# Kernel tuning notes

Measured on AMD Instinct MI355X. Metric: run time of the kernel, lower is better.

The kernel has to match this reference:

```python
import jax, jax.numpy as jnp
import numpy as np

# Module hyperparameters (init_kwargs)
DIM = 512
NUM_HEADS = 8
ALPHA = 0.5
WS = 2                       # window_size
HEAD_DIM = DIM // NUM_HEADS  # 64
L_HEADS = int(NUM_HEADS * ALPHA)      # 4 low-freq heads
L_DIM = L_HEADS * HEAD_DIM            # 256
H_HEADS = NUM_HEADS - L_HEADS         # 4 high-freq heads
H_DIM = H_HEADS * HEAD_DIM            # 256
SCALE = HEAD_DIM ** -0.5

B, HH, WW = 8, 64, 64  # batch, feature-map height/width


def setup_inputs() -> dict:
    key = jax.random.key(0)
    ks = jax.random.split(key, 7)
    s = 0.02  # weight init scale
    return {
        "x": jax.random.normal(ks[0], (B, HH * WW, DIM), jnp.float32),
        "h_qkv_w": jax.random.normal(ks[1], (DIM, 3 * H_DIM), jnp.float32) * s,
        "h_proj_w": jax.random.normal(ks[2], (H_DIM, H_DIM), jnp.float32) * s,
        "h_proj_b": jnp.zeros((H_DIM,), jnp.float32),
        "l_q_w": jax.random.normal(ks[3], (DIM, L_DIM), jnp.float32) * s,
        "l_kv_w": jax.random.normal(ks[4], (DIM, 2 * L_DIM), jnp.float32) * s,
        "l_proj_w": jax.random.normal(ks[5], (L_DIM, L_DIM), jnp.float32) * s,
        "l_proj_b": jnp.zeros((L_DIM,), jnp.float32),
        "H_in": HH,
        "W_in": WW,
    }


def _hilo_forward(x, h_qkv_w, h_proj_w, h_proj_b, l_q_w, l_kv_w, l_proj_w, l_proj_b, H, W):
    Bx, N, C = x.shape
    xi = x.reshape(Bx, H, W, C)
    hg, wg = H // WS, W // WS
    G = hg * wg  # number of windows

    # ---- Hi-Fi: window-partitioned local attention ----
    # [B, hg, WS, wg, WS, C] -> [B, G, WS*WS, C]
    xw = xi.reshape(Bx, hg, WS, wg, WS, C).transpose(0, 1, 3, 2, 4, 5).reshape(Bx, G, WS * WS, C)
    qkv = (xw @ h_qkv_w).reshape(Bx, G, WS * WS, 3, H_HEADS, HEAD_DIM)
    q, k, v = jnp.moveaxis(qkv, 3, 0)
    attn = jax.nn.softmax(jnp.einsum('bgnhd,bgmhd->bghnm', q, k) * SCALE, axis=-1)
    o = jnp.einsum('bghnm,bgmhd->bgnhd', attn, v).reshape(Bx, hg, wg, WS, WS, H_DIM)
    o = o.transpose(0, 1, 3, 2, 4, 5).reshape(Bx, H, W, H_DIM)
    hifi = o @ h_proj_w + h_proj_b  # [B, H, W, H_DIM]

    # ---- Lo-Fi: global attention over avg-pooled keys/values ----
    q = (x @ l_q_w).reshape(Bx, N, L_HEADS, HEAD_DIM).transpose(0, 2, 1, 3)  # [B, lh, N, d]
    # AvgPool2d(kernel=WS, stride=WS): mean over each WS x WS window
    xp = xi.reshape(Bx, hg, WS, wg, WS, C).mean(axis=(2, 4)).reshape(Bx, G, C)
    kv = (xp @ l_kv_w).reshape(Bx, G, 2, L_HEADS, HEAD_DIM)
    k, v = jnp.moveaxis(kv, 2, 0)  # [B, G, lh, d]
    attn = jax.nn.softmax(jnp.einsum('bhnd,bmhd->bhnm', q, k) * SCALE, axis=-1)
    lo = jnp.einsum('bhnm,bmhd->bnhd', attn, v).reshape(Bx, H, W, L_DIM)
    lofi = lo @ l_proj_w + l_proj_b  # [B, H, W, L_DIM]

    return jnp.concatenate([hifi, lofi], axis=-1).reshape(Bx, N, C)


def reference(x, h_qkv_w, h_proj_w, h_proj_b, l_q_w, l_kv_w, l_proj_w, l_proj_b, H_in, W_in):
    return _hilo_forward(x, h_qkv_w, h_proj_w, h_proj_b, l_q_w, l_kv_w, l_proj_w, l_proj_b, H_in, W_in)
```

## Files before the change

kernel.cpp:

```cpp
#include <hip/hip_runtime.h>


typedef __bf16 bf16;
typedef __attribute__((ext_vector_type(8))) __bf16 bf16x8;
typedef __attribute__((ext_vector_type(4))) __bf16 bf16x4;
typedef __attribute__((ext_vector_type(4))) float f32x4;

#define SCALE 0.125f

__device__ __forceinline__ void gload_lds16(const bf16* g, bf16* l) {
    __builtin_amdgcn_global_load_lds(
        (const __attribute__((address_space(1))) void*)g,
        (__attribute__((address_space(3))) void*)l, 16, 0, 0);
}

template <int BM, int BN, bool OUT_BF16, bool BIAS>
__global__ __launch_bounds__(256, 2) void gemm_nt_k(
    const bf16* __restrict__ A, const bf16* __restrict__ Bm,
    void* __restrict__ C, const float* __restrict__ bias,
    int K, int lda, int ldb, int ldc,
    long sAb, long sBb, long sCb, int nh, long sAh, long sBh, long sCh)
{
    constexpr int BK = 32;
    constexpr int FM = BM / 32;
    constexpr int FN = BN / 32;
    constexpr int AL = BM / 64;
    constexpr int BL = BN / 64;

    __shared__ bf16 As[BM * BK];
    __shared__ bf16 Bs[BN * BK];

    const int tid = threadIdx.x, lane = tid & 63, wv = tid >> 6;
    const int wm = wv >> 1, wn = wv & 1;

    const int z = blockIdx.z;
    const int bz = z / nh, hz = z % nh;
    A  += (size_t)bz * sAb + (size_t)hz * sAh;
    Bm += (size_t)bz * sBb + (size_t)hz * sBh;
    const size_t coff = (size_t)bz * sCb + (size_t)hz * sCh;

    const int rowBase = blockIdx.x * BM;
    const int colBase = blockIdx.y * BN;

    const int lrow = lane >> 2;
    const int lkb  = (((lane & 3) ^ ((lane >> 3) & 3))) * 8;

    f32x4 acc[FM][FN] = {};

    const int nkt = K / BK;
    for (int kt = 0; kt < nkt; ++kt) {
#pragma unroll
        for (int i = 0; i < AL; ++i) {
            const int wl = wv * AL + i;
            const int r  = wl * 16 + lrow;
            gload_lds16(A + (size_t)(rowBase + r) * lda + kt * BK + lkb,
                        &As[wl * 512]);
        }
#pragma unroll
        for (int i = 0; i < BL; ++i) {
            const int wl = wv * BL + i;
            const int r  = wl * 16 + lrow;
            gload_lds16(Bm + (size_t)(colBase + r) * ldb + kt * BK + lkb,
                        &Bs[wl * 512]);
        }
        __syncthreads();

        bf16x8 af[FM], bfr[FN];
#pragma unroll
        for (int fm = 0; fm < FM; ++fm) {
            const int row = wm * (FM * 16) + fm * 16 + (lane & 15);
            const int sl  = (lane >> 4) ^ ((row >> 1) & 3);
            af[fm] = *(const bf16x8*)&As[row * BK + sl * 8];
        }
#pragma unroll
        for (int fn = 0; fn < FN; ++fn) {
            const int row = wn * (FN * 16) + fn * 16 + (lane & 15);
            const int sl  = (lane >> 4) ^ ((row >> 1) & 3);
            bfr[fn] = *(const bf16x8*)&Bs[row * BK + sl * 8];
        }
#pragma unroll
        for (int fm = 0; fm < FM; ++fm)
#pragma unroll
            for (int fn = 0; fn < FN; ++fn)
                acc[fm][fn] = __builtin_amdgcn_mfma_f32_16x16x32_bf16(
                    af[fm], bfr[fn], acc[fm][fn], 0, 0, 0);
        __syncthreads();
    }

#pragma unroll
    for (int fm = 0; fm < FM; ++fm) {
#pragma unroll
        for (int fn = 0; fn < FN; ++fn) {
#pragma unroll
            for (int j = 0; j < 4; ++j) {
                const int row = rowBase + wm * (FM * 16) + fm * 16 + (lane >> 4) * 4 + j;
                const int col = colBase + wn * (FN * 16) + fn * 16 + (lane & 15);
                float v = acc[fm][fn][j];
                if (BIAS) v += bias[col];
                if (OUT_BF16)
                    ((bf16*)C)[coff + (size_t)row * ldc + col] = (bf16)v;
                else
                    ((float*)C)[coff + (size_t)row * ldc + col] = v;
            }
        }
    }
}

__global__ __launch_bounds__(256) void convert_x(const float* __restrict__ x,
                                                 bf16* __restrict__ xb)
{
    const size_t i = ((size_t)blockIdx.x * 256 + threadIdx.x) * 8;
    const float4 a = *(const float4*)(x + i);
    const float4 b = *(const float4*)(x + i + 4);
    bf16x8 o;
    o[0] = (bf16)a.x; o[1] = (bf16)a.y; o[2] = (bf16)a.z; o[3] = (bf16)a.w;
    o[4] = (bf16)b.x; o[5] = (bf16)b.y; o[6] = (bf16)b.z; o[7] = (bf16)b.w;
    *(bf16x8*)(xb + i) = o;
}

__global__ __launch_bounds__(256) void transpose_w(const float* __restrict__ in,
                                                   bf16* __restrict__ out,
                                                   int K, int N)
{
    const int i = blockIdx.x * 256 + threadIdx.x;
    if (i >= K * N) return;
    const int n = i / K, k = i % K;
    out[i] = (bf16)in[(size_t)k * N + n];
}

__global__ __launch_bounds__(256) void avgpool_x(const float* __restrict__ x,
                                                 bf16* __restrict__ xp)
{
    const int i = blockIdx.x * 256 + threadIdx.x;
    const int c4 = i & 127;
    const int g  = (i >> 7) & 1023;
    const int b  = i >> 17;
    const int gy = g >> 5, gx = g & 31;
    const float* base = x + ((size_t)b * 4096 + gy * 128 + gx * 2) * 512 + c4 * 4;
    const float4 a0 = *(const float4*)(base);
    const float4 a1 = *(const float4*)(base + 512);
    const float4 a2 = *(const float4*)(base + 64 * 512);
    const float4 a3 = *(const float4*)(base + 65 * 512);
    bf16x4 o;
    o[0] = (bf16)((a0.x + a1.x + a2.x + a3.x) * 0.25f);
    o[1] = (bf16)((a0.y + a1.y + a2.y + a3.y) * 0.25f);
    o[2] = (bf16)((a0.z + a1.z + a2.z + a3.z) * 0.25f);
    o[3] = (bf16)((a0.w + a1.w + a2.w + a3.w) * 0.25f);
    *(bf16x4*)(xp + ((size_t)b * 1024 + g) * 512 + c4 * 4) = o;
}

__global__ __launch_bounds__(256) void win_attn(const bf16* __restrict__ qkv,
                                                bf16* __restrict__ o_h)
{
    __shared__ float p_lds[4][64];
    const int wv = threadIdx.x >> 6, lane = threadIdx.x & 63;
    const int w = blockIdx.x * 4 + wv;
    const int b = w >> 10, g = w & 1023;
    const int gy = g >> 5, gx = g & 31;
    int t[4];
    t[0] = gy * 128 + gx * 2; t[1] = t[0] + 1; t[2] = t[0] + 64; t[3] = t[0] + 65;

    const int h = lane >> 4, n = (lane >> 2) & 3, m = lane & 3;
    const bf16* qp = qkv + ((size_t)b * 4096 + t[n]) * 768 + h * 64;
    const bf16* kp = qkv + ((size_t)b * 4096 + t[m]) * 768 + 256 + h * 64;
    float s = 0.f;
#pragma unroll
    for (int i = 0; i < 8; ++i) {
        const bf16x8 a = *(const bf16x8*)(qp + i * 8);
        const bf16x8 c = *(const bf16x8*)(kp + i * 8);
#pragma unroll
        for (int j = 0; j < 8; ++j) s += (float)a[j] * (float)c[j];
    }
    s *= SCALE;
    float mx = fmaxf(s, __shfl_xor(s, 1)); mx = fmaxf(mx, __shfl_xor(mx, 2));
    const float e = __expf(s - mx);
    float sum = e + __shfl_xor(e, 1); sum = sum + __shfl_xor(sum, 2);
    p_lds[wv][lane] = e / sum;
    __syncthreads();

#pragma unroll
    for (int hn = 0; hn < 16; ++hn) {
        const int hh = hn >> 2, nn = hn & 3;
        float o = 0.f;
#pragma unroll
        for (int mm = 0; mm < 4; ++mm) {
            const float p = p_lds[wv][hh * 16 + nn * 4 + mm];
            o += p * (float)qkv[((size_t)b * 4096 + t[mm]) * 768 + 512 + hh * 64 + lane];
        }
        o_h[((size_t)b * 4096 + t[nn]) * 256 + hh * 64 + lane] = (bf16)o;
    }
}

__global__ __launch_bounds__(256) void make_kT(const bf16* __restrict__ kv,
                                               bf16* __restrict__ kT)
{
    const int i = blockIdx.x * 256 + threadIdx.x;
    const int e = i & 7, s = (i >> 3) & 7, key = (i >> 6) & 1023;
    const int h = (i >> 16) & 3, b = i >> 18;
    kT[i] = kv[((size_t)(b * 1024 + key)) * 512 + h * 64 + (((s ^ (key & 7)) << 3) | e)];
}

__global__ __launch_bounds__(256) void make_vT(const bf16* __restrict__ kv,
                                               bf16* __restrict__ vT)
{
    const int i = blockIdx.x * 256 + threadIdx.x;
    const int e = i & 7, s = (i >> 3) & 7, c = (i >> 6) & 15;
    const int d = (i >> 10) & 63, h = (i >> 16) & 3, b = i >> 18;
    const int g = c * 64 + (((s ^ (d & 7)) << 3) | e);
    vT[i] = kv[((size_t)(b * 1024 + g)) * 512 + 256 + h * 64 + d];
}

__global__ __launch_bounds__(256, 2) void lofi_attn(
    const bf16* __restrict__ q_l, const bf16* __restrict__ kT,
    const bf16* __restrict__ vT, bf16* __restrict__ lo)
{
    __shared__ bf16 Ks[64][64];
    __shared__ bf16 Vs[64][64];
    __shared__ bf16 Ps[4][16][72];

    const int lane = threadIdx.x & 63, wv = threadIdx.x >> 6;
    const int g16 = lane >> 4, l15 = lane & 15;
    const int bh = blockIdx.y, b = bh >> 2, h = bh & 3;

    const int qrow = blockIdx.x * 64 + wv * 16 + l15;
    const bf16* qbase = q_l + ((size_t)b * 4096 + qrow) * 256 + h * 64;
    const bf16x8 qf0 = *(const bf16x8*)(qbase + g16 * 8);
    const bf16x8 qf1 = *(const bf16x8*)(qbase + 32 + g16 * 8);

    const bf16* kTb = kT + (size_t)bh * 1024 * 64;
    const bf16* vTb = vT + (size_t)bh * 64 * 1024;

    f32x4 of[4] = {};
    float m = -1e30f, l = 0.f;

    for (int kc = 0; kc < 16; ++kc) {
        const int r0 = wv * 16;
#pragma unroll
        for (int i = 0; i < 2; ++i) {
            gload_lds16(kTb + ((size_t)(kc * 64 + r0 + i * 8)) * 64 + lane * 8,
                        &Ks[r0 + i * 8][0]);
            gload_lds16(vTb + ((size_t)(r0 + i * 8 + (lane >> 3))) * 1024
                            + kc * 64 + (lane & 7) * 8,
                        &Vs[r0 + i * 8][0]);
        }
        __syncthreads();

        f32x4 s[4];
#pragma unroll
        for (int nf = 0; nf < 4; ++nf) {
            const int key = nf * 16 + l15;
            const int f = key & 7;
            const bf16x8 ka0 = *(const bf16x8*)&Ks[key][((g16) ^ f) * 8];
            const bf16x8 ka1 = *(const bf16x8*)&Ks[key][((4 + g16) ^ f) * 8];
            f32x4 a = {};
            a = __builtin_amdgcn_mfma_f32_16x16x32_bf16(ka0, qf0, a, 0, 0, 0);
            a = __builtin_amdgcn_mfma_f32_16x16x32_bf16(ka1, qf1, a, 0, 0, 0);
            s[nf] = a;
        }

        float cm = -1e30f;
#pragma unroll
        for (int nf = 0; nf < 4; ++nf)
#pragma unroll
            for (int j = 0; j < 4; ++j) {
                s[nf][j] *= SCALE;
                cm = fmaxf(cm, s[nf][j]);
            }
        cm = fmaxf(cm, __shfl_xor(cm, 16));
        cm = fmaxf(cm, __shfl_xor(cm, 32));
        const float newm = fmaxf(m, cm);
        const float corr = __expf(m - newm);
        float cs = 0.f;
#pragma unroll
        for (int nf = 0; nf < 4; ++nf) {
            bf16x4 pw;
#pragma unroll
            for (int j = 0; j < 4; ++j) {
                const float p = __expf(s[nf][j] - newm);
                cs += p;
                pw[j] = (bf16)p;
            }
            *(bf16x4*)&Ps[wv][l15][nf * 16 + g16 * 4] = pw;
        }
        cs += __shfl_xor(cs, 16);
        cs += __shfl_xor(cs, 32);
        l = l * corr + cs;
        m = newm;

        float corr_t[4];
#pragma unroll
        for (int j = 0; j < 4; ++j) corr_t[j] = __shfl(corr, g16 * 4 + j);
#pragma unroll
        for (int df = 0; df < 4; ++df)
#pragma unroll
            for (int j = 0; j < 4; ++j) of[df][j] *= corr_t[j];

        const bf16x8 pa0 = *(const bf16x8*)&Ps[wv][l15][g16 * 8];
        const bf16x8 pa1 = *(const bf16x8*)&Ps[wv][l15][32 + g16 * 8];
#pragma unroll
        for (int df = 0; df < 4; ++df) {
            const int d = df * 16 + l15;
            const int f = d & 7;
            const bf16x8 vb0 = *(const bf16x8*)&Vs[d][((g16) ^ f) * 8];
            const bf16x8 vb1 = *(const bf16x8*)&Vs[d][((4 + g16) ^ f) * 8];
            of[df] = __builtin_amdgcn_mfma_f32_16x16x32_bf16(pa0, vb0, of[df], 0, 0, 0);
            of[df] = __builtin_amdgcn_mfma_f32_16x16x32_bf16(pa1, vb1, of[df], 0, 0, 0);
        }
        __syncthreads();
    }

    const float linv = 1.0f / l;
    float linv_t[4];
#pragma unroll
    for (int j = 0; j < 4; ++j) linv_t[j] = __shfl(linv, g16 * 4 + j);
    const int orow0 = blockIdx.x * 64 + wv * 16;
#pragma unroll
    for (int df = 0; df < 4; ++df)
#pragma unroll
        for (int j = 0; j < 4; ++j) {
            const int row = orow0 + g16 * 4 + j;
            lo[((size_t)b * 4096 + row) * 256 + h * 64 + df * 16 + l15] =
                (bf16)(of[df][j] * linv_t[j]);
        }
}

extern "C" void kernel_launch(void* const* d_in, const int* in_sizes, int n_in,
                              void* d_out, int out_size, void* d_ws, size_t ws_size,
                              hipStream_t stream)
{
    const float* x        = (const float*)d_in[0];
    const float* h_qkv_w  = (const float*)d_in[1];
    const float* h_proj_w = (const float*)d_in[2];
    const float* h_proj_b = (const float*)d_in[3];
    const float* l_q_w    = (const float*)d_in[4];
    const float* l_kv_w   = (const float*)d_in[5];
    const float* l_proj_w = (const float*)d_in[6];
    const float* l_proj_b = (const float*)d_in[7];
    float* out = (float*)d_out;

    char* ws = (char*)d_ws;
    bf16*  xb    = (bf16*)(ws + 0);
    bf16*  wqkvT = (bf16*)(ws + 33554432);
    bf16*  whpT  = (bf16*)(ws + 34340864);
    bf16*  wlqT  = (bf16*)(ws + 34471936);
    bf16*  wlkvT = (bf16*)(ws + 34734080);
    bf16*  wlpT  = (bf16*)(ws + 35258368);
    bf16*  qkv   = (bf16*)(ws + 35389440);
    bf16*  o_h   = (bf16*)(ws + 85721088);
    bf16*  kT    = (bf16*)(ws + 85721088);
    bf16*  vT    = (bf16*)(ws + 89915392);
    bf16*  q_l   = (bf16*)(ws + 102498304);
    bf16*  xp    = (bf16*)(ws + 119275520);
    bf16*  kv    = (bf16*)(ws + 127664128);
    bf16*  lo    = (bf16*)(ws + 136052736);

    convert_x<<<8192, 256, 0, stream>>>(x, xb);
    transpose_w<<<1536, 256, 0, stream>>>(h_qkv_w, wqkvT, 512, 768);
    transpose_w<<<256, 256, 0, stream>>>(h_proj_w, whpT, 256, 256);
    transpose_w<<<512, 256, 0, stream>>>(l_q_w, wlqT, 512, 256);
    transpose_w<<<1024, 256, 0, stream>>>(l_kv_w, wlkvT, 512, 512);
    transpose_w<<<256, 256, 0, stream>>>(l_proj_w, wlpT, 256, 256);

    gemm_nt_k<128, 128, true, false><<<dim3(256, 6, 1), 256, 0, stream>>>(
        xb, wqkvT, qkv, nullptr, 512, 512, 512, 768, 0, 0, 0, 1, 0, 0, 0);
    win_attn<<<2048, 256, 0, stream>>>(qkv, o_h);
    gemm_nt_k<128, 128, false, true><<<dim3(256, 2, 1), 256, 0, stream>>>(
        o_h, whpT, out, h_proj_b, 256, 256, 256, 512, 0, 0, 0, 1, 0, 0, 0);

    gemm_nt_k<128, 128, true, false><<<dim3(256, 2, 1), 256, 0, stream>>>(
        xb, wlqT, q_l, nullptr, 512, 512, 512, 256, 0, 0, 0, 1, 0, 0, 0);
    avgpool_x<<<4096, 256, 0, stream>>>(x, xp);
    gemm_nt_k<128, 128, true, false><<<dim3(64, 4, 1), 256, 0, stream>>>(
        xp, wlkvT, kv, nullptr, 512, 512, 512, 512, 0, 0, 0, 1, 0, 0, 0);
    make_kT<<<8192, 256, 0, stream>>>(kv, kT);
    make_vT<<<8192, 256, 0, stream>>>(kv, vT);

    lofi_attn<<<dim3(64, 32), 256, 0, stream>>>(q_l, kT, vT, lo);

    gemm_nt_k<128, 128, false, true><<<dim3(256, 2, 1), 256, 0, stream>>>(
        lo, wlpT, out + 256, l_proj_b, 256, 256, 256, 512, 0, 0, 0, 1, 0, 0, 0);
}
```

Measured before the change: 337.2 us.

## Double-buffer lofi attention K/V tiles, double queries per wave, remap blocks per XCD

The lofi attention kernel now double-buffers K/V tiles in LDS, issuing the next chunk's global-to-LDS loads before computing on the current one. This leaves one barrier per iteration instead of two. Each wave handles two 16-row query groups, so each loaded K/V tile is reused twice, and the grid becomes a 1D launch of 1024 blocks mapped so that one XCD's blocks share the same batch-head K/V data. The two K/V transpose kernels are merged into one launch. The cost is more LDS and registers per block, which may reduce occupancy.

```diff
diff --git a/kernel.cpp b/kernel.cpp
--- a/kernel.cpp
+++ b/kernel.cpp
@@ -191,137 +191,171 @@
     }
 }
 
-__global__ __launch_bounds__(256) void make_kT(const bf16* __restrict__ kv,
-                                               bf16* __restrict__ kT)
-{
-    const int i = blockIdx.x * 256 + threadIdx.x;
-    const int e = i & 7, s = (i >> 3) & 7, key = (i >> 6) & 1023;
-    const int h = (i >> 16) & 3, b = i >> 18;
-    kT[i] = kv[((size_t)(b * 1024 + key)) * 512 + h * 64 + (((s ^ (key & 7)) << 3) | e)];
-}
-
-__global__ __launch_bounds__(256) void make_vT(const bf16* __restrict__ kv,
-                                               bf16* __restrict__ vT)
-{
-    const int i = blockIdx.x * 256 + threadIdx.x;
-    const int e = i & 7, s = (i >> 3) & 7, c = (i >> 6) & 15;
-    const int d = (i >> 10) & 63, h = (i >> 16) & 3, b = i >> 18;
-    const int g = c * 64 + (((s ^ (d & 7)) << 3) | e);
-    vT[i] = kv[((size_t)(b * 1024 + g)) * 512 + 256 + h * 64 + d];
+__global__ __launch_bounds__(256) void make_kvT(const bf16* __restrict__ kv,
+                                                bf16* __restrict__ kT,
+                                                bf16* __restrict__ vT)
+{
+    const int idx = blockIdx.x * 256 + threadIdx.x;
+    if (idx < 2097152) {
+        const int i = idx;
+        const int e = i & 7, s = (i >> 3) & 7, key = (i >> 6) & 1023;
+        const int h = (i >> 16) & 3, b = i >> 18;
+        kT[i] = kv[((size_t)(b * 1024 + key)) * 512 + h * 64 + (((s ^ (key & 7)) << 3) | e)];
+    } else {
+        const int i = idx - 2097152;
+        const int e = i & 7, s = (i >> 3) & 7, c = (i >> 6) & 15;
+        const int d = (i >> 10) & 63, h = (i >> 16) & 3, b = i >> 18;
+        const int g = c * 64 + (((s ^ (d & 7)) << 3) | e);
+        vT[i] = kv[((size_t)(b * 1024 + g)) * 512 + 256 + h * 64 + d];
+    }
 }
 
 __global__ __launch_bounds__(256, 2) void lofi_attn(
     const bf16* __restrict__ q_l, const bf16* __restrict__ kT,
     const bf16* __restrict__ vT, bf16* __restrict__ lo)
 {
-    __shared__ bf16 Ks[64][64];
-    __shared__ bf16 Vs[64][64];
+    __shared__ bf16 Ks[2][64][64];
+    __shared__ bf16 Vs[2][64][64];
     __shared__ bf16 Ps[4][16][72];
 
     const int lane = threadIdx.x & 63, wv = threadIdx.x >> 6;
     const int g16 = lane >> 4, l15 = lane & 15;
-    const int bh = blockIdx.y, b = bh >> 2, h = bh & 3;
-
-    const int qrow = blockIdx.x * 64 + wv * 16 + l15;
-    const bf16* qbase = q_l + ((size_t)b * 4096 + qrow) * 256 + h * 64;
-    const bf16x8 qf0 = *(const bf16x8*)(qbase + g16 * 8);
-    const bf16x8 qf1 = *(const bf16x8*)(qbase + 32 + g16 * 8);
-
-    const bf16* kTb = kT + (size_t)bh * 1024 * 64;
-    const bf16* vTb = vT + (size_t)bh * 64 * 1024;
-
-    f32x4 of[4] = {};
-    float m = -1e30f, l = 0.f;
-
+
+    const int bid = blockIdx.x;
+    const int xcd = bid & 7, chunk = bid >> 3;
+    const int bh = xcd * 4 + (chunk >> 5);
+    const int qt = chunk & 31;
+    const int b = bh >> 2, h = bh & 3;
+
+    bf16x8 qf[2][2];
+#pragma unroll
+    for (int qh = 0; qh < 2; ++qh) {
+        const int qrow = qt * 128 + wv * 32 + qh * 16 + l15;
+        const bf16* qbase = q_l + ((size_t)b * 4096 + qrow) * 256 + h * 64;
+        qf[qh][0] = *(const bf16x8*)(qbase + g16 * 8);
+        qf[qh][1] = *(const bf16x8*)(qbase + 32 + g16 * 8);
+    }
+
+    const bf16* kTb = kT + (size_t)bh * 65536;
+    const bf16* vTb = vT + (size_t)bh * 65536;
+
+    f32x4 of[2][4] = {};
+    float m0 = -1e30f, l0 = 0.f, m1 = -1e30f, l1 = 0.f;
+
+    const int r0 = wv * 16;
+    const int vrow = r0 + (lane >> 3);
+    const int vke  = (lane & 7) * 8;
+
+#define STAGE(buf, kc)                                                          \
+    {                                                                           \
+        _Pragma("unroll")                                                       \
+        for (int i = 0; i < 2; ++i) {                                           \
+            gload_lds16(kTb + ((size_t)((kc) * 64 + r0 + i * 8)) * 64 + lane * 8,\
+                        &Ks[buf][r0 + i * 8][0]);                               \
+            gload_lds16(vTb + ((size_t)(vrow + i * 8)) * 1024 + (kc) * 64 + vke,\
+                        &Vs[buf][r0 + i * 8][0]);                               \
+        }                                                                       \
+    }
+
+    STAGE(0, 0);
+    __syncthreads();
+
+    int cur = 0;
     for (int kc = 0; kc < 16; ++kc) {
-        const int r0 = wv * 16;
-#pragma unroll
-        for (int i = 0; i < 2; ++i) {
-            gload_lds16(kTb + ((size_t)(kc * 64 + r0 + i * 8)) * 64 + lane * 8,
-                        &Ks[r0 + i * 8][0]);
-            gload_lds16(vTb + ((size_t)(r0 + i * 8 + (lane >> 3))) * 1024
-                            + kc * 64 + (lane & 7) * 8,
-                        &Vs[r0 + i * 8][0]);
-        }
-        __syncthreads();
-
-        f32x4 s[4];
+        if (kc < 15) STAGE(cur ^ 1, kc + 1);
+
+        f32x4 s[2][4];
 #pragma unroll
         for (int nf = 0; nf < 4; ++nf) {
             const int key = nf * 16 + l15;
             const int f = key & 7;
-            const bf16x8 ka0 = *(const bf16x8*)&Ks[key][((g16) ^ f) * 8];
-            const bf16x8 ka1 = *(const bf16x8*)&Ks[key][((4 + g16) ^ f) * 8];
-            f32x4 a = {};
-            a = __builtin_amdgcn_mfma_f32_16x16x32_bf16(ka0, qf0, a, 0, 0, 0);
-            a = __builtin_amdgcn_mfma_f32_16x16x32_bf16(ka1, qf1, a, 0, 0, 0);
-            s[nf] = a;
-        }
-
-        float cm = -1e30f;
-#pragma unroll
-        for (int nf = 0; nf < 4; ++nf)
+            const bf16x8 ka0 = *(const bf16x8*)&Ks[cur][key][(g16 ^ f) * 8];
+            const bf16x8 ka1 = *(const bf16x8*)&Ks[cur][key][((4 + g16) ^ f) * 8];
+#pragma unroll
+            for (int qh = 0; qh < 2; ++qh) {
+                f32x4 a = {};
+                a = __builtin_amdgcn_mfma_f32_16x16x32_bf16(ka0, qf[qh][0], a, 0, 0, 0);
+                a = __builtin_amdgcn_mfma_f32_16x16x32_bf16(ka1, qf[qh][1], a, 0, 0, 0);
+                s[qh][nf] = a;
+            }
+        }
+
+#pragma unroll
+        for (int qh = 0; qh < 2; ++qh) {
+            float& m = qh ? m1 : m0;
+            float& l = qh ? l1 : l0;
+
+            float cm = -1e30f;
+#pragma unroll
+            for (int nf = 0; nf < 4; ++nf)
+#pragma unroll
+                for (int j = 0; j < 4; ++j) {
+                    s[qh][nf][j] *= SCALE;
+                    cm = fmaxf(cm, s[qh][nf][j]);
+                }
+            cm = fmaxf(cm, __shfl_xor(cm, 16));
+            cm = fmaxf(cm, __shfl_xor(cm, 32));
+            const float newm = fmaxf(m, cm);
+            const float corr = __expf(m - newm);
+            float cs = 0.f;
+#pragma unroll
+            for (int nf = 0; nf < 4; ++nf) {
+                bf16x4 pw;
+#pragma unroll
+                for (int j = 0; j < 4; ++j) {
+                    const float p = __expf(s[qh][nf][j] - newm);
+                    cs += p;
+                    pw[j] = (bf16)p;
+                }
+                *(bf16x4*)&Ps[wv][l15][nf * 16 + g16 * 4] = pw;
+            }
+            cs += __shfl_xor(cs, 16);
+            cs += __shfl_xor(cs, 32);
+            l = l * corr + cs;
+            m = newm;
+
+            float corr_t[4];
+#pragma unroll
+            for (int j = 0; j < 4; ++j) corr_t[j] = __shfl(corr, g16 * 4 + j);
+#pragma unroll
+            for (int df = 0; df < 4; ++df)
+#pragma unroll
+                for (int j = 0; j < 4; ++j) of[qh][df][j] *= corr_t[j];
+
+            const bf16x8 pa0 = *(const bf16x8*)&Ps[wv][l15][g16 * 8];
+            const bf16x8 pa1 = *(const bf16x8*)&Ps[wv][l15][32 + g16 * 8];
+#pragma unroll
+            for (int df = 0; df < 4; ++df) {
+                const int d = df * 16 + l15;
+                const int f = d & 7;
+                const bf16x8 vb0 = *(const bf16x8*)&Vs[cur][d][(g16 ^ f) * 8];
+                const bf16x8 vb1 = *(const bf16x8*)&Vs[cur][d][((4 + g16) ^ f) * 8];
+                of[qh][df] = __builtin_amdgcn_mfma_f32_16x16x32_bf16(pa0, vb0, of[qh][df], 0, 0, 0);
+                of[qh][df] = __builtin_amdgcn_mfma_f32_16x16x32_bf16(pa1, vb1, of[qh][df], 0, 0, 0);
+            }
+        }
+
+        __syncthreads();
+        cur ^= 1;
+    }
+#undef STAGE
+
+#pragma unroll
+    for (int qh = 0; qh < 2; ++qh) {
+        const float linv = 1.0f / (qh ? l1 : l0);
+        float linv_t[4];
+#pragma unroll
+        for (int j = 0; j < 4; ++j) linv_t[j] = __shfl(linv, g16 * 4 + j);
+        const int orow0 = qt * 128 + wv * 32 + qh * 16;
+#pragma unroll
+        for (int df = 0; df < 4; ++df)
 #pragma unroll
             for (int j = 0; j < 4; ++j) {
-                s[nf][j] *= SCALE;
-                cm = fmaxf(cm, s[nf][j]);
+                const int row = orow0 + g16 * 4 + j;
+                lo[((size_t)b * 4096 + row) * 256 + h * 64 + df * 16 + l15] =
+                    (bf16)(of[qh][df][j] * linv_t[j]);
             }
-        cm = fmaxf(cm, __shfl_xor(cm, 16));
-        cm = fmaxf(cm, __shfl_xor(cm, 32));
-        const float newm = fmaxf(m, cm);
-        const float corr = __expf(m - newm);
-        float cs = 0.f;
-#pragma unroll
-        for (int nf = 0; nf < 4; ++nf) {
-            bf16x4 pw;
-#pragma unroll
-            for (int j = 0; j < 4; ++j) {
-                const float p = __expf(s[nf][j] - newm);
-                cs += p;
-                pw[j] = (bf16)p;
-            }
-            *(bf16x4*)&Ps[wv][l15][nf * 16 + g16 * 4] = pw;
-        }
-        cs += __shfl_xor(cs, 16);
-        cs += __shfl_xor(cs, 32);
-        l = l * corr + cs;
-        m = newm;
-
-        float corr_t[4];
-#pragma unroll
-        for (int j = 0; j < 4; ++j) corr_t[j] = __shfl(corr, g16 * 4 + j);
-#pragma unroll
-        for (int df = 0; df < 4; ++df)
-#pragma unroll
-            for (int j = 0; j < 4; ++j) of[df][j] *= corr_t[j];
-
-        const bf16x8 pa0 = *(const bf16x8*)&Ps[wv][l15][g16 * 8];
-        const bf16x8 pa1 = *(const bf16x8*)&Ps[wv][l15][32 + g16 * 8];
-#pragma unroll
-        for (int df = 0; df < 4; ++df) {
-            const int d = df * 16 + l15;
-            const int f = d & 7;
-            const bf16x8 vb0 = *(const bf16x8*)&Vs[d][((g16) ^ f) * 8];
-            const bf16x8 vb1 = *(const bf16x8*)&Vs[d][((4 + g16) ^ f) * 8];
-            of[df] = __builtin_amdgcn_mfma_f32_16x16x32_bf16(pa0, vb0, of[df], 0, 0, 0);
-            of[df] = __builtin_amdgcn_mfma_f32_16x16x32_bf16(pa1, vb1, of[df], 0, 0, 0);
-        }
-        __syncthreads();
-    }
-
-    const float linv = 1.0f / l;
-    float linv_t[4];
-#pragma unroll
-    for (int j = 0; j < 4; ++j) linv_t[j] = __shfl(linv, g16 * 4 + j);
-    const int orow0 = blockIdx.x * 64 + wv * 16;
-#pragma unroll
-    for (int df = 0; df < 4; ++df)
-#pragma unroll
-        for (int j = 0; j < 4; ++j) {
-            const int row = orow0 + g16 * 4 + j;
-            lo[((size_t)b * 4096 + row) * 256 + h * 64 + df * 16 + l15] =
-                (bf16)(of[df][j] * linv_t[j]);
-        }
+    }
 }
 
 extern "C" void kernel_launch(void* const* d_in, const int* in_sizes, int n_in,
@@ -372,10 +406,9 @@
     avgpool_x<<<4096, 256, 0, stream>>>(x, xp);
     gemm_nt_k<128, 128, true, false><<<dim3(64, 4, 1), 256, 0, stream>>>(
         xp, wlkvT, kv, nullptr, 512, 512, 512, 512, 0, 0, 0, 1, 0, 0, 0);
-    make_kT<<<8192, 256, 0, stream>>>(kv, kT);
-    make_vT<<<8192, 256, 0, stream>>>(kv, vT);
-
-    lofi_attn<<<dim3(64, 32), 256, 0, stream>>>(q_l, kT, vT, lo);
+    make_kvT<<<16384, 256, 0, stream>>>(kv, kT, vT);
+
+    lofi_attn<<<1024, 256, 0, stream>>>(q_l, kT, vT, lo);
 
     gemm_nt_k<128, 128, false, true><<<dim3(256, 2, 1), 256, 0, stream>>>(
         lo, wlpT, out + 256, l_proj_b, 256, 256, 256, 512, 0, 0, 0, 1, 0, 0, 0);
```

New measurement: 340.3 us. No clear change (+0.9%).
